# Optimization experiments

Hardware: AMD Instinct MI355X
Metric: run time of the kernel (lower is better)

The kernel has to match this reference:

```python
import jax, jax.numpy as jnp
import numpy as np

D_MODEL = 1024
N_HEADS = 16
HEAD_DIM = D_MODEL // N_HEADS
Q_PROJ = D_MODEL // 2
KV_PROJ = D_MODEL
INIT_SCALE = 0.02
EPS = 1e-5


def _ln(x, g, b):
    mu = jnp.mean(x, axis=-1, keepdims=True)
    var = jnp.mean(jnp.square(x - mu), axis=-1, keepdims=True)
    return (x - mu) * jax.lax.rsqrt(var + EPS) * g + b


def setup_inputs() -> dict:
    key = jax.random.key(0)
    ks = jax.random.split(key, 8)
    B, S = 2, 2048
    x = jax.random.normal(ks[0], (B, S, D_MODEL), dtype=jnp.float32)
    W_dq = INIT_SCALE * jax.random.normal(ks[1], (D_MODEL, Q_PROJ), dtype=jnp.float32)
    W_uq = INIT_SCALE * jax.random.normal(ks[2], (Q_PROJ, D_MODEL), dtype=jnp.float32)
    W_dkv = INIT_SCALE * jax.random.normal(ks[3], (D_MODEL, KV_PROJ), dtype=jnp.float32)
    W_ukv = INIT_SCALE * jax.random.normal(ks[4], (KV_PROJ, 2 * D_MODEL), dtype=jnp.float32)
    wo = INIT_SCALE * jax.random.normal(ks[5], (D_MODEL, D_MODEL), dtype=jnp.float32)
    return {
        "x": x,
        "W_dq": W_dq, "W_uq": W_uq,
        "q_ln_g": jnp.ones((Q_PROJ,), jnp.float32), "q_ln_b": jnp.zeros((Q_PROJ,), jnp.float32),
        "W_dkv": W_dkv, "W_ukv": W_ukv,
        "kv_ln_g": jnp.ones((KV_PROJ,), jnp.float32), "kv_ln_b": jnp.zeros((KV_PROJ,), jnp.float32),
        "preq_g": jnp.ones((D_MODEL,), jnp.float32), "preq_b": jnp.zeros((D_MODEL,), jnp.float32),
        "prekv_g": jnp.ones((D_MODEL,), jnp.float32), "prekv_b": jnp.zeros((D_MODEL,), jnp.float32),
        "wo": wo,
    }


def reference(x, W_dq, W_uq, q_ln_g, q_ln_b, W_dkv, W_ukv, kv_ln_g, kv_ln_b,
              preq_g, preq_b, prekv_g, prekv_b, wo):
    B, S, D = x.shape
    H, dh = N_HEADS, HEAD_DIM
    # Q path: pre-norm -> low-rank down -> LN -> up
    x_q = _ln(x, preq_g, preq_b)
    cq = _ln(x_q @ W_dq, q_ln_g, q_ln_b)            # [B,S,D/2]
    Q = (cq @ W_uq).reshape(B, S, H, dh)             # [B,S,H,dh]
    Q = Q / jnp.sqrt(jnp.asarray(dh, x.dtype))
    # KV path: pre-norm -> compress -> LN -> up, split into K,V
    x_kv = _ln(x, prekv_g, prekv_b)
    ckv = _ln(x_kv @ W_dkv, kv_ln_g, kv_ln_b)        # [B,S,D]
    KV = ckv @ W_ukv                                 # [B,S,2D]
    K, V = jnp.split(KV, 2, axis=-1)
    K = K.reshape(B, S, H, dh)
    V = V.reshape(B, S, H, dh)
    # causal attention (scores materialized as in original)
    scores = jnp.einsum('bqhd,bkhd->bhqk', Q, K)     # [B,H,S,S]
    causal = jnp.tril(jnp.ones((S, S), dtype=bool))  # True where allowed
    scores = jnp.where(causal[None, None], scores, jnp.asarray(-jnp.inf, scores.dtype))
    attn = jax.nn.softmax(scores, axis=-1)
    out = jnp.einsum('bhqk,bkhd->bqhd', attn, V).reshape(B, S, D)
    return out @ wo.T
```

## Files before the change

kernel.cpp:

```cpp
#include <hip/hip_runtime.h>
#include <hip/hip_bf16.h>

#define SEQ   2048
#define BATCH 2
#define NROWS 4096
#define DM    1024
#define NHEAD 16
#define DH    64
#define QP    512
#define KVP   1024
#define CH    8

typedef unsigned short us;
typedef ushort4 us4;
using bf16x8 = __attribute__((ext_vector_type(8))) __bf16;
using f32x4  = __attribute__((ext_vector_type(4))) float;

__device__ __forceinline__ us f2bf(float f) {
  union { __hip_bfloat16 h; us u; } cv;
  cv.h = __float2bfloat16(f);
  return cv.u;
}
__device__ __forceinline__ float bf2f(us u) {
  union { unsigned int u32; float f; } cv;
  cv.u32 = ((unsigned int)u) << 16;
  return cv.f;
}
__device__ __forceinline__ float loadp(const void* p, long i, int isbf) {
  return isbf ? bf2f(((const us*)p)[i]) : ((const float*)p)[i];
}
__device__ __forceinline__ void async16(const void* g, void* l) {
  __builtin_amdgcn_global_load_lds((__attribute__((address_space(1))) void*)g,
                                   (__attribute__((address_space(3))) void*)l,
                                   16, 0, 0);
}

__global__ void detect_dtype(const us* __restrict__ xu, int* __restrict__ flag) {
  __shared__ int red[256];
  const int tid = threadIdx.x;
  int cnt = 0;
  for (int i = tid; i < 4096; i += 256) {
    const int e = (xu[i] >> 7) & 0xff;
    if (e == 0 || (e >= 100 && e <= 134)) cnt++;
  }
  red[tid] = cnt;
  __syncthreads();
  for (int s = 128; s; s >>= 1) {
    if (tid < s) red[tid] += red[tid + s];
    __syncthreads();
  }
  if (tid == 0) *flag = (red[0] >= 3900) ? 1 : 0;
}

struct TD { const void* in; us* out; int R, C, nt, trans; };

__global__ __launch_bounds__(256) void stage0(
    TD t0, TD t1, TD t2, TD t3, TD t4,
    float4* __restrict__ zp, int n4,
    const void* __restrict__ xin,
    const void* __restrict__ g1, const void* __restrict__ b1,
    const void* __restrict__ g2, const void* __restrict__ b2,
    us* __restrict__ out1, us* __restrict__ out2,
    const int* __restrict__ flag)
{
  __shared__ us tile[32][33];
  __shared__ float red[8];
  __shared__ float musd[2];
  const int tid = threadIdx.x;
  const int isbf = *flag;
  int lin = blockIdx.x;

  if (lin < 5120) {
    TD t = t0;
    if (lin >= t.nt) { lin -= t.nt; t = t1;
      if (lin >= t.nt) { lin -= t.nt; t = t2;
        if (lin >= t.nt) { lin -= t.nt; t = t3;
          if (lin >= t.nt) { lin -= t.nt; t = t4; } } } }
    const int ntx = t.C >> 5;
    const int by = lin / ntx, bx = lin - by * ntx;
    const int tx = tid & 31, ty = tid >> 5;
    const long r0 = (long)by * 32, c0 = (long)bx * 32;
    if (t.trans) {
#pragma unroll
      for (int i = 0; i < 32; i += 8)
        tile[ty + i][tx] = isbf ? ((const us*)t.in)[(r0 + ty + i) * t.C + c0 + tx]
                                : f2bf(((const float*)t.in)[(r0 + ty + i) * t.C + c0 + tx]);
      __syncthreads();
#pragma unroll
      for (int i = 0; i < 32; i += 8)
        t.out[(c0 + ty + i) * t.R + r0 + tx] = tile[tx][ty + i];
    } else {
#pragma unroll
      for (int i = 0; i < 32; i += 8)
        t.out[(r0 + ty + i) * t.C + c0 + tx] =
            isbf ? ((const us*)t.in)[(r0 + ty + i) * t.C + c0 + tx]
                 : f2bf(((const float*)t.in)[(r0 + ty + i) * t.C + c0 + tx]);
    }
    return;
  }
  if (lin < 6144) {
    const float4 z = {0.f, 0.f, 0.f, 0.f};
    for (int i = (lin - 5120) * 256 + tid; i < n4; i += 1024 * 256) zp[i] = z;
    return;
  }
  const long row = lin - 6144;
  float v[4];
  float s = 0.f, s2 = 0.f;
#pragma unroll
  for (int i = 0; i < 4; i++) {
    const long c = tid + i * 256;
    const float t = loadp(xin, row * 1024 + c, isbf);
    v[i] = t; s += t; s2 += t * t;
  }
#pragma unroll
  for (int off = 32; off > 0; off >>= 1) {
    s  += __shfl_down(s,  off);
    s2 += __shfl_down(s2, off);
  }
  const int wave = tid >> 6, lane = tid & 63;
  if (lane == 0) { red[wave] = s; red[4 + wave] = s2; }
  __syncthreads();
  if (tid == 0) {
    const float ts = red[0] + red[1] + red[2] + red[3];
    const float t2 = red[4] + red[5] + red[6] + red[7];
    const float mu = ts * (1.f / 1024.f);
    const float var = t2 * (1.f / 1024.f) - mu * mu;
    musd[0] = mu; musd[1] = rsqrtf(var + 1e-5f);
  }
  __syncthreads();
  const float mu = musd[0], rs = musd[1];
#pragma unroll
  for (int i = 0; i < 4; i++) {
    const long c = tid + i * 256;
    const float nrm = (v[i] - mu) * rs;
    out1[row * 1024 + c] = f2bf(nrm * loadp(g1, c, isbf) + loadp(b1, c, isbf));
    out2[row * 1024 + c] = f2bf(nrm * loadp(g2, c, isbf) + loadp(b2, c, isbf));
  }
}

template<int C>
__device__ __forceinline__ void ln_body(const us* __restrict__ in,
                                        const void* __restrict__ g, const void* __restrict__ b,
                                        us* __restrict__ out, long row, int tid, int isbf) {
  constexpr int NP = C / 256;
  float v[NP];
  float s = 0.f, s2 = 0.f;
#pragma unroll
  for (int i = 0; i < NP; i++) {
    const float t = bf2f(in[row * C + tid + i * 256]);
    v[i] = t; s += t; s2 += t * t;
  }
#pragma unroll
  for (int off = 32; off > 0; off >>= 1) {
    s  += __shfl_down(s,  off);
    s2 += __shfl_down(s2, off);
  }
  __shared__ float red[8];
  __shared__ float musd[2];
  const int wave = tid >> 6, lane = tid & 63;
  if (lane == 0) { red[wave] = s; red[4 + wave] = s2; }
  __syncthreads();
  if (tid == 0) {
    const float ts = red[0] + red[1] + red[2] + red[3];
    const float t2 = red[4] + red[5] + red[6] + red[7];
    const float mu = ts * (1.f / C);
    const float var = t2 * (1.f / C) - mu * mu;
    musd[0] = mu; musd[1] = rsqrtf(var + 1e-5f);
  }
  __syncthreads();
  const float mu = musd[0], rs = musd[1];
#pragma unroll
  for (int i = 0; i < NP; i++) {
    const long c = tid + i * 256;
    out[row * C + c] = f2bf((v[i] - mu) * rs * loadp(g, c, isbf) + loadp(b, c, isbf));
  }
}

__global__ __launch_bounds__(256) void ln_rows_pair(
    const us* __restrict__ inq, const void* __restrict__ qg, const void* __restrict__ qb,
    us* __restrict__ outq,
    const us* __restrict__ inkv, const void* __restrict__ kvg, const void* __restrict__ kvb,
    us* __restrict__ outkv,
    const int* __restrict__ flag)
{
  const int isbf = *flag;
  if (blockIdx.x < NROWS)
    ln_body<512>(inq, qg, qb, outq, blockIdx.x, threadIdx.x, isbf);
  else
    ln_body<1024>(inkv, kvg, kvb, outkv, blockIdx.x - NROWS, threadIdx.x, isbf);
}

struct GD { const us* A; const us* Bt; void* C; int N, K, nxs; float scale; int omode; };

__global__ __launch_bounds__(256) void gemm_mt(GD g0, GD g1, int nb0,
                                               const int* __restrict__ flag) {
  __shared__ us As[2][128 * 32];
  __shared__ us Bs[2][128 * 32];
  GD g;
  int lin = blockIdx.x;
  if (lin < nb0) g = g0; else { g = g1; lin -= nb0; }
  const int by = lin >> g.nxs;
  const int bx = lin - (by << g.nxs);
  const int N = g.N, K = g.K;

  const int tid  = threadIdx.x;
  const int lane = tid & 63;
  const int wave = tid >> 6;
  const int n16  = lane & 15;
  const int quad = lane >> 4;
  const long m0 = (long)by * 128;
  const long n0 = (long)bx * 128;
  const int wm = (wave >> 1) * 64;
  const int wn = (wave & 1) * 64;

  const f32x4 zero = {0.f, 0.f, 0.f, 0.f};
  f32x4 acc[4][4];
#pragma unroll
  for (int i = 0; i < 4; i++)
#pragma unroll
    for (int j = 0; j < 4; j++) acc[i][j] = zero;

  const int srow = tid >> 2;
  const int scol = (tid & 3) * 8;
  const us* Ag0 = g.A  + (m0 + srow) * K + scol;
  const us* Ag1 = g.A  + (m0 + 64 + srow) * K + scol;
  const us* Bg0 = g.Bt + (n0 + srow) * K + scol;
  const us* Bg1 = g.Bt + (n0 + 64 + srow) * K + scol;
  const int lds_off = srow * 32 + scol;

  for (int k0 = 0; k0 < K; k0 += 64) {
#pragma unroll
    for (int s = 0; s < 2; s++) {
      const int ks = k0 + s * 32;
      async16(Ag0 + ks, As[s] + lds_off);
      async16(Ag1 + ks, As[s] + 2048 + lds_off);
      async16(Bg0 + ks, Bs[s] + lds_off);
      async16(Bg1 + ks, Bs[s] + 2048 + lds_off);
    }
    __syncthreads();
#pragma unroll
    for (int s = 0; s < 2; s++) {
      bf16x8 af[4], bfv[4];
#pragma unroll
      for (int i = 0; i < 4; i++)
        af[i] = *(const bf16x8*)(As[s] + (wm + i * 16 + n16) * 32 + quad * 8);
#pragma unroll
      for (int j = 0; j < 4; j++)
        bfv[j] = *(const bf16x8*)(Bs[s] + (wn + j * 16 + n16) * 32 + quad * 8);
#pragma unroll
      for (int i = 0; i < 4; i++)
#pragma unroll
        for (int j = 0; j < 4; j++)
          acc[i][j] = __builtin_amdgcn_mfma_f32_16x16x32_bf16(af[i], bfv[j], acc[i][j], 0, 0, 0);
    }
    __syncthreads();
  }

  const bool obf = (g.omode == 1) || (g.omode == 2 && *flag != 0);
  float* Cf = (float*)g.C;
  us* Cb = (us*)g.C;
#pragma unroll
  for (int i = 0; i < 4; i++) {
    const long row = m0 + wm + i * 16 + quad * 4;
#pragma unroll
    for (int j = 0; j < 4; j++) {
      const long col = n0 + wn + j * 16 + n16;
#pragma unroll
      for (int r = 0; r < 4; r++) {
        const float v = acc[i][j][r] * g.scale;
        if (obf) Cb[(row + r) * N + col] = f2bf(v);
        else     Cf[(row + r) * N + col] = v;
      }
    }
  }
}

__global__ __launch_bounds__(256) void flash_attn(
    const us* __restrict__ Q, const us* __restrict__ KV,
    float* __restrict__ Oacc, float* __restrict__ Lacc)
{
  __shared__ us Ks[64 * 72];
  __shared__ us Vt[64 * 72];
  __shared__ us Ps[4][32 * 72];

  int lin = blockIdx.x;
  int qt = 15, nc = 0;
  for (; qt >= 0; --qt) { nc = ((2 * qt + 1) >> 3) + 1; if (lin < nc) break; lin -= nc; }
  const int kt0 = lin * CH;
  const int kt1 = min(kt0 + CH, 2 * qt + 2);

  const int h   = blockIdx.y;
  const int bb  = blockIdx.z;
  const int tid = threadIdx.x;
  const int lane = tid & 63;
  const int wave = tid >> 6;
  const int n16 = lane & 15;
  const int quad = lane >> 4;
  const int qbase = qt * 128;
  const long rowQ0 = (long)bb * SEQ;

  bf16x8 aq[2][2];
#pragma unroll
  for (int rg = 0; rg < 2; rg++) {
    const long gq = (rowQ0 + qbase + wave * 32 + rg * 16 + n16) * DM + h * DH;
    aq[rg][0] = *(const bf16x8*)(Q + gq + quad * 8);
    aq[rg][1] = *(const bf16x8*)(Q + gq + 32 + quad * 8);
  }

  const f32x4 zero = {0.f, 0.f, 0.f, 0.f};
  f32x4 oacc[2][4];
#pragma unroll
  for (int rg = 0; rg < 2; rg++)
#pragma unroll
    for (int d = 0; d < 4; d++) oacc[rg][d] = zero;
  float rsum[2] = {0.f, 0.f};

  const int kk_key = tid >> 3;
  const int kk_d8  = (tid & 7) * 8;
  const int vd  = tid & 63;
  const int vkb = (tid >> 6) * 8;

  const us* kgb = KV + (rowQ0 + kk_key) * 2048 + h * DH + kk_d8;
  const us* vgb = KV + (rowQ0 + vkb) * 2048 + KVP + h * DH + vd;

  uint4 kpre0, kpre1;
  us vraw[16];
  auto loadKV = [&](int kt) {
    const us* kg = kgb + (long)kt * (64 * 2048);
    kpre0 = *(const uint4*)kg;
    kpre1 = *(const uint4*)(kg + 32 * 2048);
    const us* vg = vgb + (long)kt * (64 * 2048);
#pragma unroll
    for (int j = 0; j < 8; j++) vraw[j] = vg[j * 2048];
    const us* vg2 = vg + 32 * 2048;
#pragma unroll
    for (int j = 0; j < 8; j++) vraw[8 + j] = vg2[j * 2048];
  };
  loadKV(kt0);

  us* Pw = Ps[wave];
  const int qw = qbase + wave * 32;

  for (int kt = kt0; kt < kt1; kt++) {
    const int kb = kt * 64;
    __syncthreads();
    *(uint4*)(Ks + kk_key * 72 + kk_d8)        = kpre0;
    *(uint4*)(Ks + (kk_key + 32) * 72 + kk_d8) = kpre1;
    {
      uint4 p0, p1;
      p0.x = (unsigned)vraw[0]  | ((unsigned)vraw[1]  << 16);
      p0.y = (unsigned)vraw[2]  | ((unsigned)vraw[3]  << 16);
      p0.z = (unsigned)vraw[4]  | ((unsigned)vraw[5]  << 16);
      p0.w = (unsigned)vraw[6]  | ((unsigned)vraw[7]  << 16);
      p1.x = (unsigned)vraw[8]  | ((unsigned)vraw[9]  << 16);
      p1.y = (unsigned)vraw[10] | ((unsigned)vraw[11] << 16);
      p1.z = (unsigned)vraw[12] | ((unsigned)vraw[13] << 16);
      p1.w = (unsigned)vraw[14] | ((unsigned)vraw[15] << 16);
      *(uint4*)(Vt + vd * 72 + vkb)      = p0;
      *(uint4*)(Vt + vd * 72 + vkb + 32) = p1;
    }
    __syncthreads();
    if (kt + 1 < kt1) loadKV(kt + 1);

    if (kb > qw + 31) continue;

    f32x4 sv[2][4];
#pragma unroll
    for (int j = 0; j < 4; j++) {
      const bf16x8 ak0 = *(const bf16x8*)(Ks + (j * 16 + n16) * 72 + quad * 8);
      const bf16x8 ak1 = *(const bf16x8*)(Ks + (j * 16 + n16) * 72 + 32 + quad * 8);
#pragma unroll
      for (int rg = 0; rg < 2; rg++) {
        f32x4 s = zero;
        s = __builtin_amdgcn_mfma_f32_16x16x32_bf16(ak0, aq[rg][0], s, 0, 0, 0);
        s = __builtin_amdgcn_mfma_f32_16x16x32_bf16(ak1, aq[rg][1], s, 0, 0, 0);
        sv[rg][j] = s;
      }
    }

#pragma unroll
    for (int rg = 0; rg < 2; rg++) {
      if (kb + 63 > qw + rg * 16) {
        const int qg = qw + rg * 16 + n16;
#pragma unroll
        for (int j = 0; j < 4; j++) {
          const int kl = kb + j * 16 + quad * 4;
#pragma unroll
          for (int r = 0; r < 4; r++)
            sv[rg][j][r] = (kl + r <= qg) ? sv[rg][j][r] : -1e30f;
        }
      }
#pragma unroll
      for (int j = 0; j < 4; j++) {
        const float p0 = __builtin_amdgcn_exp2f(sv[rg][j][0]);
        const float p1 = __builtin_amdgcn_exp2f(sv[rg][j][1]);
        const float p2 = __builtin_amdgcn_exp2f(sv[rg][j][2]);
        const float p3 = __builtin_amdgcn_exp2f(sv[rg][j][3]);
        rsum[rg] += (p0 + p1) + (p2 + p3);
        us4 pk;
        pk.x = f2bf(p0); pk.y = f2bf(p1); pk.z = f2bf(p2); pk.w = f2bf(p3);
        *(us4*)(Pw + (rg * 16 + n16) * 72 + j * 16 + quad * 4) = pk;
      }
    }
    __asm__ volatile("s_waitcnt lgkmcnt(0)" ::: "memory");

#pragma unroll
    for (int rg = 0; rg < 2; rg++)
#pragma unroll
      for (int kc = 0; kc < 2; kc++) {
        const bf16x8 ap = *(const bf16x8*)(Pw + (rg * 16 + n16) * 72 + kc * 32 + quad * 8);
#pragma unroll
        for (int d = 0; d < 4; d++) {
          const bf16x8 bv = *(const bf16x8*)(Vt + (d * 16 + n16) * 72 + kc * 32 + quad * 8);
          oacc[rg][d] = __builtin_amdgcn_mfma_f32_16x16x32_bf16(ap, bv, oacc[rg][d], 0, 0, 0);
        }
      }
  }

#pragma unroll
  for (int rg = 0; rg < 2; rg++) {
    float rs = rsum[rg];
    rs += __shfl_xor(rs, 16);
    rs += __shfl_xor(rs, 32);
    const long rw0 = rowQ0 + qbase + wave * 32 + rg * 16;
    if (quad == 0)
      atomicAdd(&Lacc[(rw0 + n16) * NHEAD + h], rs);
#pragma unroll
    for (int r = 0; r < 4; r++) {
      float* dst = Oacc + (rw0 + quad * 4 + r) * DM + h * DH + n16;
#pragma unroll
      for (int d = 0; d < 4; d++)
        atomicAdd(dst + d * 16, oacc[rg][d][r]);
    }
  }
}

__global__ __launch_bounds__(256) void flash_combine(
    const float* __restrict__ Oacc, const float* __restrict__ Lacc,
    us* __restrict__ O)
{
  __shared__ float invl[NHEAD];
  const long row = blockIdx.x;
  const int tid = threadIdx.x;
  if (tid < NHEAD) invl[tid] = 1.f / Lacc[row * NHEAD + tid];
  __syncthreads();
#pragma unroll
  for (int i = 0; i < 4; i++) {
    const int col = tid + i * 256;
    O[row * DM + col] = f2bf(Oacc[row * DM + col] * invl[col >> 6]);
  }
}

extern "C" void kernel_launch(void* const* d_in, const int* in_sizes, int n_in,
                              void* d_out, int out_size, void* d_ws, size_t ws_size,
                              hipStream_t stream) {
  const void* x      = d_in[0];
  const void* Wdq    = d_in[1];
  const void* Wuq    = d_in[2];
  const void* qg     = d_in[3];
  const void* qb     = d_in[4];
  const void* Wdkv   = d_in[5];
  const void* Wukv   = d_in[6];
  const void* kvg    = d_in[7];
  const void* kvb    = d_in[8];
  const void* preqg  = d_in[9];
  const void* preqb  = d_in[10];
  const void* prekvg = d_in[11];
  const void* prekvb = d_in[12];
  const void* wo     = d_in[13];

  char* ws = (char*)d_ws;
  const long MB = 1 << 20;
  int* flag   = (int*)ws;
  us* wdq_t   = (us*)(ws + 1 * MB);
  us* wuq_t   = (us*)(ws + 2 * MB);
  us* wdkv_t  = (us*)(ws + 3 * MB);
  us* wukv_t  = (us*)(ws + 5 * MB);
  us* wo_c    = (us*)(ws + 9 * MB);
  us* xq      = (us*)(ws + 11 * MB);
  us* xkv     = (us*)(ws + 19 * MB);
  float* Oacc = (float*)(ws + 27 * MB);
  float* Lacc = (float*)(ws + 43 * MB);
  us* obuf    = (us*)(ws + 43 * MB + 256 * 1024);
  us* tq_bf   = obuf;
  us* cq      = (us*)(ws + 43 * MB + 256 * 1024 + 8 * MB);
  us* qbuf    = (us*)(ws + 43 * MB + 256 * 1024 + 12 * MB);
  us* tkv_bf  = qbuf;
  us* ckv     = (us*)(ws + 43 * MB + 256 * 1024 + 20 * MB);
  us* kv      = (us*)(ws + 43 * MB + 256 * 1024 + 28 * MB);

  detect_dtype<<<1, 256, 0, stream>>>((const us*)x, flag);

  {
    TD t0 = { Wdq,  wdq_t,  1024,  512,  512, 1 };
    TD t1 = { Wuq,  wuq_t,   512, 1024,  512, 1 };
    TD t2 = { Wdkv, wdkv_t, 1024, 1024, 1024, 1 };
    TD t3 = { Wukv, wukv_t, 1024, 2048, 2048, 1 };
    TD t4 = { wo,   wo_c,   1024, 1024, 1024, 0 };
    const int n4 = (16 * 1024 * 1024 + 256 * 1024) / 16;
    stage0<<<10240, 256, 0, stream>>>(t0, t1, t2, t3, t4,
                                      (float4*)Oacc, n4,
                                      x, preqg, preqb, prekvg, prekvb, xq, xkv, flag);
  }

  {
    GD g0 = { xq,  wdq_t,  tq_bf,   512, 1024, 2, 1.f, 1 };
    GD g1 = { xkv, wdkv_t, tkv_bf, 1024, 1024, 3, 1.f, 1 };
    gemm_mt<<<384, 256, 0, stream>>>(g0, g1, 128, flag);
  }

  ln_rows_pair<<<2 * NROWS, 256, 0, stream>>>(tq_bf, qg, qb, cq, tkv_bf, kvg, kvb, ckv, flag);

  {
    GD g0 = { cq,  wuq_t,  qbuf, 1024,  512, 3, 0.125f * 1.44269504f, 1 };
    GD g1 = { ckv, wukv_t, kv,   2048, 1024, 4, 1.f, 1 };
    gemm_mt<<<768, 256, 0, stream>>>(g0, g1, 256, flag);
  }

  flash_attn<<<dim3(40, NHEAD, BATCH), 256, 0, stream>>>(qbuf, kv, Oacc, Lacc);
  flash_combine<<<NROWS, 256, 0, stream>>>(Oacc, Lacc, obuf);

  {
    GD g0 = { obuf, wo_c, d_out, 1024, 1024, 3, 1.f, 2 };
    gemm_mt<<<256, 256, 0, stream>>>(g0, g0, 256, flag);
  }
}
```

Before: 282.6 us.

## Fold mid-LayerNorm into GEMM epilogues and emit transposed V from up-projection

Removes the separate LayerNorm kernel over the low-rank projections. The down-projection GEMM now accumulates per-row sum and sum-of-squares with atomics. The up-projection GEMM applies the normalization algebraically, using gamma folded into the transposed weights plus precomputed column sums u and c. The KV up-projection also writes V directly in transposed layout, so flash attention loads it with vector loads instead of strided gathers. The trade-offs are atomic traffic, a one-pass variance (E[x²]-mu²) that can be less accurate, and bf16 rounding of the raw GEMM output before normalization.

```diff
diff --git a/kernel.cpp b/kernel.cpp
--- a/kernel.cpp
+++ b/kernel.cpp
@@ -35,9 +35,12 @@
                                    16, 0, 0);
 }
 
-__global__ void detect_dtype(const us* __restrict__ xu, int* __restrict__ flag) {
+__global__ void detect_dtype(const us* __restrict__ xu, int* __restrict__ flag,
+                             float4* __restrict__ zsmall, int nz4) {
   __shared__ int red[256];
   const int tid = threadIdx.x;
+  const float4 z = {0.f, 0.f, 0.f, 0.f};
+  for (int i = tid; i < nz4; i += 256) zsmall[i] = z;
   int cnt = 0;
   for (int i = tid; i < 4096; i += 256) {
     const int e = (xu[i] >> 7) & 0xff;
@@ -52,7 +55,8 @@
   if (tid == 0) *flag = (red[0] >= 3900) ? 1 : 0;
 }
 
-struct TD { const void* in; us* out; int R, C, nt, trans; };
+struct TD { const void* in; us* out; int R, C, nt, trans;
+            const void* g; const void* b; float* u; float* c; };
 
 __global__ __launch_bounds__(256) void stage0(
     TD t0, TD t1, TD t2, TD t3, TD t4,
@@ -86,9 +90,26 @@
         tile[ty + i][tx] = isbf ? ((const us*)t.in)[(r0 + ty + i) * t.C + c0 + tx]
                                 : f2bf(((const float*)t.in)[(r0 + ty + i) * t.C + c0 + tx]);
       __syncthreads();
-#pragma unroll
-      for (int i = 0; i < 32; i += 8)
-        t.out[(c0 + ty + i) * t.R + r0 + tx] = tile[tx][ty + i];
+      if (t.g) {
+        const float gw = loadp(t.g, r0 + tx, isbf);
+#pragma unroll
+        for (int i = 0; i < 32; i += 8)
+          t.out[(c0 + ty + i) * t.R + r0 + tx] = f2bf(bf2f(tile[tx][ty + i]) * gw);
+        if (ty == 0) {
+          float up = 0.f, cp = 0.f;
+          for (int r = 0; r < 32; r++) {
+            const float w = bf2f(tile[r][tx]);
+            up += loadp(t.g, r0 + r, isbf) * w;
+            cp += loadp(t.b, r0 + r, isbf) * w;
+          }
+          atomicAdd(&t.u[c0 + tx], up);
+          atomicAdd(&t.c[c0 + tx], cp);
+        }
+      } else {
+#pragma unroll
+        for (int i = 0; i < 32; i += 8)
+          t.out[(c0 + ty + i) * t.R + r0 + tx] = tile[tx][ty + i];
+      }
     } else {
 #pragma unroll
       for (int i = 0; i < 32; i += 8)
@@ -138,59 +159,8 @@
   }
 }
 
-template<int C>
-__device__ __forceinline__ void ln_body(const us* __restrict__ in,
-                                        const void* __restrict__ g, const void* __restrict__ b,
-                                        us* __restrict__ out, long row, int tid, int isbf) {
-  constexpr int NP = C / 256;
-  float v[NP];
-  float s = 0.f, s2 = 0.f;
-#pragma unroll
-  for (int i = 0; i < NP; i++) {
-    const float t = bf2f(in[row * C + tid + i * 256]);
-    v[i] = t; s += t; s2 += t * t;
-  }
-#pragma unroll
-  for (int off = 32; off > 0; off >>= 1) {
-    s  += __shfl_down(s,  off);
-    s2 += __shfl_down(s2, off);
-  }
-  __shared__ float red[8];
-  __shared__ float musd[2];
-  const int wave = tid >> 6, lane = tid & 63;
-  if (lane == 0) { red[wave] = s; red[4 + wave] = s2; }
-  __syncthreads();
-  if (tid == 0) {
-    const float ts = red[0] + red[1] + red[2] + red[3];
-    const float t2 = red[4] + red[5] + red[6] + red[7];
-    const float mu = ts * (1.f / C);
-    const float var = t2 * (1.f / C) - mu * mu;
-    musd[0] = mu; musd[1] = rsqrtf(var + 1e-5f);
-  }
-  __syncthreads();
-  const float mu = musd[0], rs = musd[1];
-#pragma unroll
-  for (int i = 0; i < NP; i++) {
-    const long c = tid + i * 256;
-    out[row * C + c] = f2bf((v[i] - mu) * rs * loadp(g, c, isbf) + loadp(b, c, isbf));
-  }
-}
-
-__global__ __launch_bounds__(256) void ln_rows_pair(
-    const us* __restrict__ inq, const void* __restrict__ qg, const void* __restrict__ qb,
-    us* __restrict__ outq,
-    const us* __restrict__ inkv, const void* __restrict__ kvg, const void* __restrict__ kvb,
-    us* __restrict__ outkv,
-    const int* __restrict__ flag)
-{
-  const int isbf = *flag;
-  if (blockIdx.x < NROWS)
-    ln_body<512>(inq, qg, qb, outq, blockIdx.x, threadIdx.x, isbf);
-  else
-    ln_body<1024>(inkv, kvg, kvb, outkv, blockIdx.x - NROWS, threadIdx.x, isbf);
-}
-
-struct GD { const us* A; const us* Bt; void* C; int N, K, nxs; float scale; int omode; };
+struct GD { const us* A; const us* Bt; void* C; int N, K, nxs; float scale; int omode;
+            float* S1; float* S2; const float* u; const float* cv; us* C2; };
 
 __global__ __launch_bounds__(256) void gemm_mt(GD g0, GD g1, int nb0,
                                                const int* __restrict__ flag) {
@@ -256,9 +226,100 @@
     __syncthreads();
   }
 
-  const bool obf = (g.omode == 1) || (g.omode == 2 && *flag != 0);
+  const int om = g.omode;
+  us* Cb = (us*)g.C;
+
+  if (om == 4) {
+    float s1a[4][4], s2a[4][4];
+#pragma unroll
+    for (int i = 0; i < 4; i++)
+#pragma unroll
+      for (int r = 0; r < 4; r++) { s1a[i][r] = 0.f; s2a[i][r] = 0.f; }
+#pragma unroll
+    for (int i = 0; i < 4; i++) {
+      const long row = m0 + wm + i * 16 + quad * 4;
+#pragma unroll
+      for (int j = 0; j < 4; j++) {
+        const long col = n0 + wn + j * 16 + n16;
+#pragma unroll
+        for (int r = 0; r < 4; r++) {
+          const float v = acc[i][j][r] * g.scale;
+          Cb[(row + r) * N + col] = f2bf(v);
+          s1a[i][r] += v;
+          s2a[i][r] += v * v;
+        }
+      }
+    }
+#pragma unroll
+    for (int i = 0; i < 4; i++)
+#pragma unroll
+      for (int r = 0; r < 4; r++) {
+        float a = s1a[i][r], b = s2a[i][r];
+#pragma unroll
+        for (int off = 1; off < 16; off <<= 1) {
+          a += __shfl_xor(a, off);
+          b += __shfl_xor(b, off);
+        }
+        if (n16 == 0) {
+          const long row = m0 + wm + i * 16 + quad * 4 + r;
+          atomicAdd(&g.S1[row], a);
+          atomicAdd(&g.S2[row], b);
+        }
+      }
+    return;
+  }
+
+  if (om == 5 || om == 6) {
+    const float invK = 1.f / (float)K;
+    float rsr[4][4], mur[4][4];
+#pragma unroll
+    for (int i = 0; i < 4; i++) {
+      const long row = m0 + wm + i * 16 + quad * 4;
+#pragma unroll
+      for (int r = 0; r < 4; r++) {
+        const float s1 = g.S1[row + r];
+        const float s2 = g.S2[row + r];
+        const float mu = s1 * invK;
+        const float var = s2 * invK - mu * mu;
+        const float rs = rsqrtf(var + 1e-5f);
+        rsr[i][r] = rs;
+        mur[i][r] = mu * rs;
+      }
+    }
+    const bool vhalf = (om == 6) && (n0 >= 1024);
+#pragma unroll
+    for (int i = 0; i < 4; i++) {
+      const long rowb = m0 + wm + i * 16 + quad * 4;
+#pragma unroll
+      for (int j = 0; j < 4; j++) {
+        const long col = n0 + wn + j * 16 + n16;
+        const float uu = g.u[col];
+        const float cc = g.cv[col];
+        if (!vhalf) {
+          const int nst = (om == 6) ? 1024 : N;
+#pragma unroll
+          for (int r = 0; r < 4; r++) {
+            const float v = g.scale * (rsr[i][r] * acc[i][j][r] - mur[i][r] * uu + cc);
+            Cb[(rowb + r) * nst + col] = f2bf(v);
+          }
+        } else {
+          const int bbq = (int)(rowb >> 11);
+          const int key = (int)(rowb & 2047);
+          const int dimg = (int)col - 1024;
+          us4 pk;
+          pk.x = f2bf(g.scale * (rsr[i][0] * acc[i][j][0] - mur[i][0] * uu + cc));
+          pk.y = f2bf(g.scale * (rsr[i][1] * acc[i][j][1] - mur[i][1] * uu + cc));
+          pk.z = f2bf(g.scale * (rsr[i][2] * acc[i][j][2] - mur[i][2] * uu + cc));
+          pk.w = f2bf(g.scale * (rsr[i][3] * acc[i][j][3] - mur[i][3] * uu + cc));
+          *(us4*)(g.C2 + ((long)(bbq * 1024 + dimg)) * 2048 + key) = pk;
+        }
+      }
+    }
+    return;
+  }
+
+  const bool obf = (om == 1) || (om == 2 && *flag != 0);
   float* Cf = (float*)g.C;
-  us* Cb = (us*)g.C;
 #pragma unroll
   for (int i = 0; i < 4; i++) {
     const long row = m0 + wm + i * 16 + quad * 4;
@@ -276,7 +337,8 @@
 }
 
 __global__ __launch_bounds__(256) void flash_attn(
-    const us* __restrict__ Q, const us* __restrict__ KV,
+    const us* __restrict__ Kbuf, const us* __restrict__ VT,
+    const us* __restrict__ Q,
     float* __restrict__ Oacc, float* __restrict__ Lacc)
 {
   __shared__ us Ks[64 * 72];
@@ -320,21 +382,17 @@
   const int vd  = tid & 63;
   const int vkb = (tid >> 6) * 8;
 
-  const us* kgb = KV + (rowQ0 + kk_key) * 2048 + h * DH + kk_d8;
-  const us* vgb = KV + (rowQ0 + vkb) * 2048 + KVP + h * DH + vd;
-
-  uint4 kpre0, kpre1;
-  us vraw[16];
+  const us* kgb = Kbuf + (rowQ0 + kk_key) * 1024 + h * DH + kk_d8;
+  const us* vtb = VT + ((long)bb * 1024 + h * DH + vd) * 2048;
+
+  uint4 kpre0, kpre1, vpre0, vpre1;
   auto loadKV = [&](int kt) {
-    const us* kg = kgb + (long)kt * (64 * 2048);
+    const us* kg = kgb + (long)kt * (64 * 1024);
     kpre0 = *(const uint4*)kg;
-    kpre1 = *(const uint4*)(kg + 32 * 2048);
-    const us* vg = vgb + (long)kt * (64 * 2048);
-#pragma unroll
-    for (int j = 0; j < 8; j++) vraw[j] = vg[j * 2048];
-    const us* vg2 = vg + 32 * 2048;
-#pragma unroll
-    for (int j = 0; j < 8; j++) vraw[8 + j] = vg2[j * 2048];
+    kpre1 = *(const uint4*)(kg + 32 * 1024);
+    const us* vg = vtb + kt * 64 + vkb;
+    vpre0 = *(const uint4*)vg;
+    vpre1 = *(const uint4*)(vg + 32);
   };
   loadKV(kt0);
 
@@ -346,19 +404,8 @@
     __syncthreads();
     *(uint4*)(Ks + kk_key * 72 + kk_d8)        = kpre0;
     *(uint4*)(Ks + (kk_key + 32) * 72 + kk_d8) = kpre1;
-    {
-      uint4 p0, p1;
-      p0.x = (unsigned)vraw[0]  | ((unsigned)vraw[1]  << 16);
-      p0.y = (unsigned)vraw[2]  | ((unsigned)vraw[3]  << 16);
-      p0.z = (unsigned)vraw[4]  | ((unsigned)vraw[5]  << 16);
-      p0.w = (unsigned)vraw[6]  | ((unsigned)vraw[7]  << 16);
-      p1.x = (unsigned)vraw[8]  | ((unsigned)vraw[9]  << 16);
-      p1.y = (unsigned)vraw[10] | ((unsigned)vraw[11] << 16);
-      p1.z = (unsigned)vraw[12] | ((unsigned)vraw[13] << 16);
-      p1.w = (unsigned)vraw[14] | ((unsigned)vraw[15] << 16);
-      *(uint4*)(Vt + vd * 72 + vkb)      = p0;
-      *(uint4*)(Vt + vd * 72 + vkb + 32) = p1;
-    }
+    *(uint4*)(Vt + vd * 72 + vkb)              = vpre0;
+    *(uint4*)(Vt + vd * 72 + vkb + 32)         = vpre1;
     __syncthreads();
     if (kt + 1 < kt1) loadKV(kt + 1);
 
@@ -471,7 +518,17 @@
 
   char* ws = (char*)d_ws;
   const long MB = 1 << 20;
-  int* flag   = (int*)ws;
+  int* flag = (int*)ws;
+  float* S1q  = (float*)(ws + 4096);
+  float* S2q  = S1q + 4096;
+  float* S1kv = S2q + 4096;
+  float* S2kv = S1kv + 4096;
+  float* u2q  = S2kv + 4096;
+  float* c2q  = u2q + 1024;
+  float* u2kv = c2q + 1024;
+  float* c2kv = u2kv + 2048;
+  const int nz4 = (4 * 4096 + 2 * 1024 + 2 * 2048) / 4;
+
   us* wdq_t   = (us*)(ws + 1 * MB);
   us* wuq_t   = (us*)(ws + 2 * MB);
   us* wdkv_t  = (us*)(ws + 3 * MB);
@@ -483,20 +540,19 @@
   float* Lacc = (float*)(ws + 43 * MB);
   us* obuf    = (us*)(ws + 43 * MB + 256 * 1024);
   us* tq_bf   = obuf;
-  us* cq      = (us*)(ws + 43 * MB + 256 * 1024 + 8 * MB);
-  us* qbuf    = (us*)(ws + 43 * MB + 256 * 1024 + 12 * MB);
-  us* tkv_bf  = qbuf;
-  us* ckv     = (us*)(ws + 43 * MB + 256 * 1024 + 20 * MB);
-  us* kv      = (us*)(ws + 43 * MB + 256 * 1024 + 28 * MB);
-
-  detect_dtype<<<1, 256, 0, stream>>>((const us*)x, flag);
+  us* qbuf    = (us*)(ws + 43 * MB + 256 * 1024 + 8 * MB);
+  us* tkv_bf  = (us*)(ws + 43 * MB + 256 * 1024 + 16 * MB);
+  us* Kbuf    = (us*)(ws + 43 * MB + 256 * 1024 + 24 * MB);
+  us* VT      = (us*)(ws + 43 * MB + 256 * 1024 + 32 * MB);
+
+  detect_dtype<<<1, 256, 0, stream>>>((const us*)x, flag, (float4*)S1q, nz4);
 
   {
-    TD t0 = { Wdq,  wdq_t,  1024,  512,  512, 1 };
-    TD t1 = { Wuq,  wuq_t,   512, 1024,  512, 1 };
-    TD t2 = { Wdkv, wdkv_t, 1024, 1024, 1024, 1 };
-    TD t3 = { Wukv, wukv_t, 1024, 2048, 2048, 1 };
-    TD t4 = { wo,   wo_c,   1024, 1024, 1024, 0 };
+    TD t0 = { Wdq,  wdq_t,  1024,  512,  512, 1, nullptr, nullptr, nullptr, nullptr };
+    TD t1 = { Wuq,  wuq_t,   512, 1024,  512, 1, qg,  qb,  u2q,  c2q  };
+    TD t2 = { Wdkv, wdkv_t, 1024, 1024, 1024, 1, nullptr, nullptr, nullptr, nullptr };
+    TD t3 = { Wukv, wukv_t, 1024, 2048, 2048, 1, kvg, kvb, u2kv, c2kv };
+    TD t4 = { wo,   wo_c,   1024, 1024, 1024, 0, nullptr, nullptr, nullptr, nullptr };
     const int n4 = (16 * 1024 * 1024 + 256 * 1024) / 16;
     stage0<<<10240, 256, 0, stream>>>(t0, t1, t2, t3, t4,
                                       (float4*)Oacc, n4,
@@ -504,24 +560,25 @@
   }
 
   {
-    GD g0 = { xq,  wdq_t,  tq_bf,   512, 1024, 2, 1.f, 1 };
-    GD g1 = { xkv, wdkv_t, tkv_bf, 1024, 1024, 3, 1.f, 1 };
+    GD g0 = { xq,  wdq_t,  tq_bf,   512, 1024, 2, 1.f, 4, S1q,  S2q,  nullptr, nullptr, nullptr };
+    GD g1 = { xkv, wdkv_t, tkv_bf, 1024, 1024, 3, 1.f, 4, S1kv, S2kv, nullptr, nullptr, nullptr };
     gemm_mt<<<384, 256, 0, stream>>>(g0, g1, 128, flag);
   }
 
-  ln_rows_pair<<<2 * NROWS, 256, 0, stream>>>(tq_bf, qg, qb, cq, tkv_bf, kvg, kvb, ckv, flag);
-
   {
-    GD g0 = { cq,  wuq_t,  qbuf, 1024,  512, 3, 0.125f * 1.44269504f, 1 };
-    GD g1 = { ckv, wukv_t, kv,   2048, 1024, 4, 1.f, 1 };
+    GD g0 = { tq_bf,  wuq_t,  qbuf, 1024,  512, 3, 0.125f * 1.44269504f, 5,
+              S1q,  S2q,  u2q,  c2q,  nullptr };
+    GD g1 = { tkv_bf, wukv_t, Kbuf, 2048, 1024, 4, 1.f, 6,
+              S1kv, S2kv, u2kv, c2kv, VT };
     gemm_mt<<<768, 256, 0, stream>>>(g0, g1, 256, flag);
   }
 
-  flash_attn<<<dim3(40, NHEAD, BATCH), 256, 0, stream>>>(qbuf, kv, Oacc, Lacc);
+  flash_attn<<<dim3(40, NHEAD, BATCH), 256, 0, stream>>>(Kbuf, VT, qbuf, Oacc, Lacc);
   flash_combine<<<NROWS, 256, 0, stream>>>(Oacc, Lacc, obuf);
 
   {
-    GD g0 = { obuf, wo_c, d_out, 1024, 1024, 3, 1.f, 2 };
+    GD g0 = { obuf, wo_c, d_out, 1024, 1024, 3, 1.f, 2,
+              nullptr, nullptr, nullptr, nullptr, nullptr };
     gemm_mt<<<256, 256, 0, stream>>>(g0, g0, 256, flag);
   }
 }
```

Result: slower. 288.8 us (+2.2%).
